# Optimization experiments

Hardware: AMD Instinct MI355X
Metric: run time of the kernel (lower is better)

## Reference

```python
import jax, jax.numpy as jnp
import numpy as np

N, E, H, ED, DD, TD = 40000, 640000, 128, 32, 32, 128
INPUT_CH = 2 * H + ED + DD  # 320


def setup_inputs() -> dict:
    key = jax.random.key(0)
    ks = jax.random.split(key, 14)
    s = 0.02  # param init scale
    return {
        "h": jax.random.normal(ks[0], (N, H), jnp.float32),
        "pos": jax.random.normal(ks[1], (N, 3), jnp.float32),
        "edge_attr": jax.random.normal(ks[2], (E, ED), jnp.float32),
        "dist": jax.random.normal(ks[3], (E, DD), jnp.float32),
        "time_emb": jax.random.normal(ks[4], (1, TD), jnp.float32),
        # time_mlp: SiLU -> Linear(time_dim, 2*hidden)
        "tW": jax.random.normal(ks[5], (TD, 2 * H), jnp.float32) * s,
        "tb": jnp.zeros((2 * H,), jnp.float32),
        # input_lin: Linear(input_ch, hidden)
        "iW": jax.random.normal(ks[6], (INPUT_CH, H), jnp.float32) * s,
        "ib": jnp.zeros((H,), jnp.float32),
        # coord_mlp: Linear(H,H) -> SiLU -> Linear(H,1,bias=False)
        "c1W": jax.random.normal(ks[7], (H, H), jnp.float32) * s,
        "c1b": jnp.zeros((H,), jnp.float32),
        "c2W": jax.random.normal(ks[8], (H, 1), jnp.float32) * s,
        # CoorsNorm learned scale, init 0.01
        "cn_scale": jnp.full((1,), 0.01, jnp.float32),
        "edge_index": jax.random.randint(ks[9], (2, E), 0, N, jnp.int64),
    }


def reference(h, pos, edge_attr, dist, time_emb, tW, tb, iW, ib, c1W, c1b, c2W, cn_scale, edge_index):
    row, col = edge_index[0], edge_index[1]
    # gather edge endpoint features: [E, 2H+ED+DD]
    h_input = jnp.concatenate([h[row], h[col], edge_attr, dist], axis=1)
    # CoorsNorm(scale_init=0.01): normalize relative coords, learned scale
    coord_diff = pos[row] - pos[col]  # [E, 3]
    nrm = jnp.linalg.norm(coord_diff, axis=-1, keepdims=True)
    coord_diff = coord_diff / jnp.clip(nrm, 1e-8) * cn_scale
    # FiLM params from time embedding
    t = jax.nn.silu(time_emb) @ tW + tb  # [1, 2H]
    shift, scale = jnp.split(t, 2, axis=1)
    # input_lin -> LayerNorm (no affine, eps=1e-6) -> modulate
    x = h_input @ iW + ib  # [E, H]
    mu = jnp.mean(x, axis=-1, keepdims=True)
    var = jnp.var(x, axis=-1, keepdims=True)
    x = (x - mu) * jax.lax.rsqrt(var + 1e-6)
    x = x * (1.0 + scale) + shift
    # coord_mlp -> tanh gate
    inv = jnp.tanh(jax.nn.silu(x @ c1W + c1b) @ c2W)  # [E, 1]
    trans = coord_diff * inv  # [E, 3]
    # scatter-add into per-node coordinate updates
    agg = jax.ops.segment_sum(trans, row, num_segments=pos.shape[0])
    return pos + agg
```

## Files before the change

kernel.cpp:

```cpp
#include <hip/hip_runtime.h>
#include <hip/hip_bf16.h>
#include <stdint.h>

#define NN 40000
#define EE 640000
#define HD 128
#define TDIM 128
#define TB 128
#define NTILES (EE / TB)
#define GRID 512

typedef short  s16x8 __attribute__((ext_vector_type(8)));
typedef float  f32x2 __attribute__((ext_vector_type(2)));
typedef float  f32x4 __attribute__((ext_vector_type(4)));
typedef unsigned int u32x4 __attribute__((ext_vector_type(4)));
typedef unsigned short u16;
typedef unsigned int   u32;

#define PSCL 8.0f
#define PDSC 0.125f

__device__ __forceinline__ u32 cvtpk(float lo, float hi) {
  u32 r; asm("v_cvt_pk_bf16_f32 %0, %1, %2" : "=v"(r) : "v"(lo), "v"(hi)); return r;
}
__device__ __forceinline__ u16 f2b(float f) {
  union { float f; u32 u; } x; x.f = f;
  u32 r = x.u + 0x7fffu + ((x.u >> 16) & 1u);
  return (u16)(r >> 16);
}

__global__ void prep_film_kernel(const float* __restrict__ te, const float* __restrict__ tW,
                                 const float* __restrict__ tb, float* __restrict__ film) {
  __shared__ float s[TDIM];
  int t = threadIdx.x;
  if (t < TDIM) { float v = te[t]; s[t] = v * __builtin_amdgcn_rcpf(1.f + __expf(-v)); }
  __syncthreads();
  float acc = tb[t];
  #pragma unroll 8
  for (int k = 0; k < TDIM; ++k) acc = fmaf(s[k], tW[k * 256 + t], acc);
  film[t] = (t >= 128) ? (1.f + acc) : acc;
}

__global__ void prep_weights_kernel(const float* __restrict__ iW,
                                    const float* __restrict__ c1W,
                                    const float* __restrict__ film,
                                    const float* __restrict__ c1b,
                                    u16* __restrict__ wPt,
                                    u16* __restrict__ wadWt,
                                    u16* __restrict__ c1Wt,
                                    float* __restrict__ biasp) {
  int b = blockIdx.x, t = threadIdx.x;
  if (b < 128) {
    int idx = b * 256 + t;
    int c = idx >> 7, k = idx & 127;
    wPt[idx] = f2b(iW[((c >> 7) * 128 + k) * HD + (c & 127)]);
  } else if (b < 160) {
    int idx = (b - 128) * 256 + t;
    int j = idx & 7, l15 = (idx >> 3) & 15, n = (idx >> 7) & 7, lg = (idx >> 10) & 3, ks = idx >> 12;
    int row = n * 16 + l15;
    int k = ks * 32 + lg * 8 + j;
    wadWt[idx] = f2b(iW[(256 + k) * HD + row]);
  } else if (b < 224) {
    int idx = (b - 160) * 256 + t;
    int j = idx & 7, l15 = (idx >> 3) & 15, n = (idx >> 7) & 7, lg = (idx >> 10) & 3, kq = idx >> 12;
    int row = n * 16 + l15;
    int ch = (kq * 2 + (j >> 2)) * 16 + lg * 4 + (j & 3);
    c1Wt[idx] = f2b(film[128 + ch] * c1W[ch * HD + row]);
  } else if (t < 128) {
    float acc = c1b[t];
    #pragma unroll 8
    for (int k = 0; k < 128; ++k) acc = fmaf(film[k], c1W[k * HD + t], acc);
    biasp[t] = acc;
  }
}

__global__ __launch_bounds__(256) void prep_P_kernel(const float* __restrict__ h,
                                                     const u16* __restrict__ wPt,
                                                     const float* __restrict__ ib,
                                                     const float* __restrict__ pos,
                                                     u32* __restrict__ P,
                                                     float* __restrict__ out) {
  __shared__ u16 sWp[256][136];
  __shared__ float sib[HD];
  int t = threadIdx.x;
  {
    int ci = blockIdx.x * 192 + t;
    if (t < 192) out[ci] = pos[ci];
  }
  if (t < 128) sib[t] = ib[t];
  {
    const u16* src = wPt + t * 128;
    #pragma unroll
    for (int i = 0; i < 16; ++i)
      *(uint4*)&sWp[t][i * 8] = *(const uint4*)(src + i * 8);
  }
  int wave = t >> 6, lane = t & 63, l15 = lane & 15, lg = lane >> 4;
  int node = blockIdx.x * 64 + wave * 16 + l15;
  uint4 hb[4];
  const float* hr = h + (size_t)node * HD + lg * 8;
  #pragma unroll
  for (int c = 0; c < 4; ++c) {
    float4 a = *(const float4*)(hr + c * 32);
    float4 b = *(const float4*)(hr + c * 32 + 4);
    hb[c].x = cvtpk(a.x, a.y); hb[c].y = cvtpk(a.z, a.w);
    hb[c].z = cvtpk(b.x, b.y); hb[c].w = cvtpk(b.z, b.w);
  }
  __syncthreads();
  f32x4 acc[16];
  #pragma unroll
  for (int n = 0; n < 16; ++n) acc[n] = (f32x4){0.f, 0.f, 0.f, 0.f};
  #pragma unroll
  for (int c = 0; c < 4; ++c) {
    s16x8 bF = *(const s16x8*)&hb[c];
    #pragma unroll
    for (int n = 0; n < 16; ++n) {
      s16x8 aF = *(const s16x8*)&sWp[n * 16 + l15][c * 32 + lg * 8];
      acc[n] = __builtin_amdgcn_mfma_f32_16x16x32_bf16(aF, bF, acc[n], 0, 0, 0);
    }
  }
  u32* dst = P + (size_t)node * 64;
  #pragma unroll
  for (int n = 0; n < 16; ++n) {
    int side = n >> 3;
    int cb = (n & 7) * 16 + lg * 4;
    float a0 = acc[n][0], a1 = acc[n][1], a2 = acc[n][2], a3 = acc[n][3];
    if (side == 0) { a0 += sib[cb]; a1 += sib[cb + 1]; a2 += sib[cb + 2]; a3 += sib[cb + 3]; }
    u32 w = __builtin_amdgcn_cvt_pk_fp8_f32(PSCL * a0, PSCL * a1, 0, false);
    w = __builtin_amdgcn_cvt_pk_fp8_f32(PSCL * a2, PSCL * a3, w, true);
    dst[side * 32 + lg * 8 + (n & 7)] = w;
  }
}

struct PfS {
  int ri, ci;
  float4 a0, a1, d0, d1;
  float p0x, p0y, p0z, p1x, p1y, p1z;
};

__global__ __launch_bounds__(512, 4) void edge_kernel(
    const float* __restrict__ pos,
    const float* __restrict__ edge_attr,
    const float* __restrict__ dist,
    const float* __restrict__ c2w,
    const float* __restrict__ cn_scale,
    const int*   __restrict__ eidx,
    const u32*   __restrict__ P,
    const u16*   __restrict__ wadWt,
    const u16*   __restrict__ c1Wt,
    const float* __restrict__ biasp,
    float*       __restrict__ out)
{
  __shared__ u16   sW1[8192];
  __shared__ u16   sW2[16384];
  __shared__ float sC1b[HD];
  __shared__ float sC2w[HD];

  const int t    = threadIdx.x;
  const int lane = t & 63;
  const int wave = t >> 6;
  const int l15  = lane & 15;
  const int lg   = lane >> 4;
  const int wv   = wave * 16 + l15;

  if (t < HD) { sC1b[t] = biasp[t]; sC2w[t] = c2w[t]; }
  {
    const uint4* s1 = (const uint4*)wadWt;
    uint4* d1 = (uint4*)sW1;
    #pragma unroll
    for (int i = 0; i < 2; ++i) d1[t + i * 512] = s1[t + i * 512];
    const uint4* s2 = (const uint4*)c1Wt;
    uint4* d2 = (uint4*)sW2;
    #pragma unroll
    for (int i = 0; i < 4; ++i) d2[t + i * 512] = s2[t + i * 512];
  }

  const float cns = cn_scale[0];
  const int bbase = lg * 2048 + l15 * 16;

  auto pf_idx_ad = [&](PfS& p, int tile) {
    int e = tile * TB + wv;
    p.ri = eidx[e];
    p.ci = eidx[EE + e];
    const float* pa = edge_attr + (size_t)e * 32 + lg * 8;
    const float* pd = dist      + (size_t)e * 32 + lg * 8;
    p.a0 = *(const float4*)(pa); p.a1 = *(const float4*)(pa + 4);
    p.d0 = *(const float4*)(pd); p.d1 = *(const float4*)(pd + 4);
  };
  auto pf_pos = [&](PfS& p) {
    p.p0x = pos[p.ri * 3 + 0]; p.p0y = pos[p.ri * 3 + 1]; p.p0z = pos[p.ri * 3 + 2];
    p.p1x = pos[p.ci * 3 + 0]; p.p1y = pos[p.ci * 3 + 1]; p.p1z = pos[p.ci * 3 + 2];
  };

  PfS A, B;
  pf_idx_ad(A, blockIdx.x);
  pf_pos(A);

  uint4 pra0, pra1, pca0, pca1;
  {
    const u32* pr = P + (size_t)A.ri * 64 + lg * 8;
    const u32* pc = P + (size_t)A.ci * 64 + 32 + lg * 8;
    pra0 = *(const uint4*)(pr); pra1 = *(const uint4*)(pr + 4);
    pca0 = *(const uint4*)(pc); pca1 = *(const uint4*)(pc + 4);
  }

  __syncthreads();

  for (int tile = blockIdx.x; tile < NTILES; tile += GRID) {
    int tn = tile + GRID; if (tn >= NTILES) tn = tile;

    pf_idx_ad(B, tn);

    uint4 ef0, ef1;
    ef0.x = cvtpk(A.a0.x, A.a0.y); ef0.y = cvtpk(A.a0.z, A.a0.w);
    ef0.z = cvtpk(A.a1.x, A.a1.y); ef0.w = cvtpk(A.a1.z, A.a1.w);
    ef1.x = cvtpk(A.d0.x, A.d0.y); ef1.y = cvtpk(A.d0.z, A.d0.w);
    ef1.z = cvtpk(A.d1.x, A.d1.y); ef1.w = cvtpk(A.d1.z, A.d1.w);

    f32x4 acc[8];
    #pragma unroll
    for (int n = 0; n < 8; ++n) acc[n] = (f32x4){0.f, 0.f, 0.f, 0.f};
    #pragma unroll
    for (int ks = 0; ks < 2; ++ks) {
      s16x8 bF = (ks == 0) ? *(const s16x8*)&ef0 : *(const s16x8*)&ef1;
      #pragma unroll
      for (int n = 0; n < 8; ++n) {
        s16x8 aF = *(const s16x8*)((const char*)sW1 + ks * 8192 + bbase + n * 256);
        acc[n] = __builtin_amdgcn_mfma_f32_16x16x32_bf16(aF, bF, acc[n], 0, 0, 0);
      }
    }

    float x[8][4];
    float s0=0.f,s1=0.f,s2=0.f,s3=0.f, q0=0.f,q1=0.f,q2=0.f,q3=0.f;
    #pragma unroll
    for (int i = 0; i < 2; ++i) {
      uint4 wa = (i == 0) ? pra0 : pra1;
      uint4 wc = (i == 0) ? pca0 : pca1;
      #pragma unroll
      for (int k = 0; k < 4; ++k) {
        int n = i * 4 + k;
        u32 aw = (k == 0) ? wa.x : (k == 1) ? wa.y : (k == 2) ? wa.z : wa.w;
        u32 cw = (k == 0) ? wc.x : (k == 1) ? wc.y : (k == 2) ? wc.z : wc.w;
        f32x2 a01 = __builtin_amdgcn_cvt_pk_f32_fp8(aw, false);
        f32x2 a23 = __builtin_amdgcn_cvt_pk_f32_fp8(aw, true);
        f32x2 c01 = __builtin_amdgcn_cvt_pk_f32_fp8(cw, false);
        f32x2 c23 = __builtin_amdgcn_cvt_pk_f32_fp8(cw, true);
        float v0 = fmaf(a01[0] + c01[0], PDSC, acc[n][0]);
        float v1 = fmaf(a01[1] + c01[1], PDSC, acc[n][1]);
        float v2 = fmaf(a23[0] + c23[0], PDSC, acc[n][2]);
        float v3 = fmaf(a23[1] + c23[1], PDSC, acc[n][3]);
        x[n][0] = v0; x[n][1] = v1; x[n][2] = v2; x[n][3] = v3;
        s0 += v0; s1 += v1; s2 += v2; s3 += v3;
        q0 = fmaf(v0,v0,q0); q1 = fmaf(v1,v1,q1);
        q2 = fmaf(v2,v2,q2); q3 = fmaf(v3,v3,q3);
      }
    }
    float sum = (s0 + s1) + (s2 + s3);
    float sq  = (q0 + q1) + (q2 + q3);
    sum += __shfl_xor(sum, 16); sum += __shfl_xor(sum, 32);
    sq  += __shfl_xor(sq,  16); sq  += __shfl_xor(sq,  32);
    float mean = sum * (1.f / 128.f);
    float var  = sq  * (1.f / 128.f) - mean * mean;
    float LA = rsqrtf(var + 1e-6f);
    float LB = -mean * LA;

    union { uint2 u2[8]; u32 w[16]; } xb;
    #pragma unroll
    for (int n = 0; n < 8; ++n) {
      float y0 = fmaf(x[n][0], LA, LB);
      float y1 = fmaf(x[n][1], LA, LB);
      float y2 = fmaf(x[n][2], LA, LB);
      float y3 = fmaf(x[n][3], LA, LB);
      xb.u2[n].x = cvtpk(y0, y1);
      xb.u2[n].y = cvtpk(y2, y3);
    }

    #pragma unroll
    for (int n = 0; n < 8; ++n) acc[n] = (f32x4){0.f, 0.f, 0.f, 0.f};
    #pragma unroll
    for (int kq = 0; kq < 4; ++kq) {
      u32x4 xw = { xb.w[4*kq], xb.w[4*kq+1], xb.w[4*kq+2], xb.w[4*kq+3] };
      s16x8 xF = __builtin_bit_cast(s16x8, xw);
      #pragma unroll
      for (int n = 0; n < 8; ++n) {
        s16x8 aF = *(const s16x8*)((const char*)sW2 + kq * 8192 + bbase + n * 256);
        acc[n] = __builtin_amdgcn_mfma_f32_16x16x32_bf16(aF, xF, acc[n], 0, 0, 0);
      }
    }

    float z0=0.f, z1=0.f, z2=0.f, z3=0.f;
    #pragma unroll
    for (int n = 0; n < 8; ++n) {
      int cb = n * 16 + lg * 4;
      f32x4 cb4 = *(const f32x4*)&sC1b[cb];
      f32x4 cw4 = *(const f32x4*)&sC2w[cb];
      float y0 = acc[n][0] + cb4[0];
      float y1 = acc[n][1] + cb4[1];
      float y2 = acc[n][2] + cb4[2];
      float y3 = acc[n][3] + cb4[3];
      z0 = fmaf(y0 * __builtin_amdgcn_rcpf(1.f + __expf(-y0)), cw4[0], z0);
      z1 = fmaf(y1 * __builtin_amdgcn_rcpf(1.f + __expf(-y1)), cw4[1], z1);
      z2 = fmaf(y2 * __builtin_amdgcn_rcpf(1.f + __expf(-y2)), cw4[2], z2);
      z3 = fmaf(y3 * __builtin_amdgcn_rcpf(1.f + __expf(-y3)), cw4[3], z3);
    }
    float z = (z0 + z1) + (z2 + z3);
    z += __shfl_xor(z, 16); z += __shfl_xor(z, 32);

    pf_pos(B);
    uint4 qra0, qra1, qca0, qca1;
    {
      const u32* pr = P + (size_t)B.ri * 64 + lg * 8;
      const u32* pc = P + (size_t)B.ci * 64 + 32 + lg * 8;
      qra0 = *(const uint4*)(pr); qra1 = *(const uint4*)(pr + 4);
      qca0 = *(const uint4*)(pc); qca1 = *(const uint4*)(pc + 4);
    }

    if (lg < 3) {
      float zc = fminf(fmaxf(z, -15.f), 15.f);
      float ez = __expf(2.f * zc);
      float inv = (ez - 1.f) * __builtin_amdgcn_rcpf(ez + 1.f);
      float dx = A.p0x - A.p1x, dy = A.p0y - A.p1y, dz = A.p0z - A.p1z;
      float nrm = sqrtf(fmaf(dx, dx, fmaf(dy, dy, dz * dz)));
      float sc  = cns * inv * __builtin_amdgcn_rcpf(fmaxf(nrm, 1e-8f));
      float d   = (lg == 0) ? dx : ((lg == 1) ? dy : dz);
      atomicAdd(out + (size_t)A.ri * 3 + lg, d * sc);
    }

    A = B;
    pra0 = qra0; pra1 = qra1;
    pca0 = qca0; pca1 = qca1;
  }
}

extern "C" void kernel_launch(void* const* d_in, const int* in_sizes, int n_in,
                              void* d_out, int out_size, void* d_ws, size_t ws_size,
                              hipStream_t stream) {
  const float* h         = (const float*)d_in[0];
  const float* pos       = (const float*)d_in[1];
  const float* edge_attr = (const float*)d_in[2];
  const float* dist      = (const float*)d_in[3];
  const float* te        = (const float*)d_in[4];
  const float* tW        = (const float*)d_in[5];
  const float* tb        = (const float*)d_in[6];
  const float* iW        = (const float*)d_in[7];
  const float* ib        = (const float*)d_in[8];
  const float* c1W       = (const float*)d_in[9];
  const float* c1b       = (const float*)d_in[10];
  const float* c2W       = (const float*)d_in[11];
  const float* cn        = (const float*)d_in[12];
  const int*   eidx      = (const int*)d_in[13];
  float* out = (float*)d_out;

  char* ws = (char*)d_ws;
  u32*   P      = (u32*)(ws);
  u16*   wPt    = (u16*)(ws + 10240000);
  u16*   wadWt  = (u16*)(ws + 10305536);
  u16*   c1Wt   = (u16*)(ws + 10321920);
  float* film   = (float*)(ws + 10354688);
  float* biasp  = (float*)(ws + 10355712);

  hipLaunchKernelGGL(prep_film_kernel,    dim3(1),    dim3(256), 0, stream, te, tW, tb, film);
  hipLaunchKernelGGL(prep_weights_kernel, dim3(225),  dim3(256), 0, stream,
                     iW, c1W, film, c1b, wPt, wadWt, c1Wt, biasp);
  hipLaunchKernelGGL(prep_P_kernel,       dim3(625),  dim3(256), 0, stream,
                     h, wPt, ib, pos, P, out);
  hipLaunchKernelGGL(edge_kernel,         dim3(GRID), dim3(512), 0, stream,
                     pos, edge_attr, dist, c2W, cn, eidx,
                     P, wadWt, c1Wt, biasp, out);
}
```

Baseline: 99.61 us.

## Switch edge MLP matmuls from bf16 to fp8 MFMA with scaled weights

Converts the edge-attribute/dist projection and the coord_mlp first layer to fp8 (e4m3) MFMA, storing weights pre-scaled by 16 in fp8 and undoing the scale after accumulation. This halves weight LDS footprint and operand register width, aiming to cut MFMA and LDS cost per edge. The grid is also raised from 512 to 768 blocks to use the freed LDS for more resident blocks. The cost is extra quantization error on the activations and weights.

```diff
diff --git a/kernel.cpp b/kernel.cpp
--- a/kernel.cpp
+++ b/kernel.cpp
@@ -8,17 +8,18 @@
 #define TDIM 128
 #define TB 128
 #define NTILES (EE / TB)
-#define GRID 512
+#define GRID 768
 
 typedef short  s16x8 __attribute__((ext_vector_type(8)));
 typedef float  f32x2 __attribute__((ext_vector_type(2)));
 typedef float  f32x4 __attribute__((ext_vector_type(4)));
-typedef unsigned int u32x4 __attribute__((ext_vector_type(4)));
 typedef unsigned short u16;
 typedef unsigned int   u32;
 
 #define PSCL 8.0f
 #define PDSC 0.125f
+#define WSCALE 16.0f
+#define WDSC 0.0625f
 
 __device__ __forceinline__ u32 cvtpk(float lo, float hi) {
   u32 r; asm("v_cvt_pk_bf16_f32 %0, %1, %2" : "=v"(r) : "v"(lo), "v"(hi)); return r;
@@ -54,18 +55,27 @@
     int idx = b * 256 + t;
     int c = idx >> 7, k = idx & 127;
     wPt[idx] = f2b(iW[((c >> 7) * 128 + k) * HD + (c & 127)]);
-  } else if (b < 160) {
-    int idx = (b - 128) * 256 + t;
-    int j = idx & 7, l15 = (idx >> 3) & 15, n = (idx >> 7) & 7, lg = (idx >> 10) & 3, ks = idx >> 12;
+  } else if (b < 144) {
+    int pidx = (b - 128) * 256 + t;
+    int idx = pidx * 2;
+    int j0 = idx & 7, l15 = (idx >> 3) & 15, n = (idx >> 7) & 7, lg = (idx >> 10) & 3, ks = idx >> 12;
     int row = n * 16 + l15;
-    int k = ks * 32 + lg * 8 + j;
-    wadWt[idx] = f2b(iW[(256 + k) * HD + row]);
-  } else if (b < 224) {
-    int idx = (b - 160) * 256 + t;
-    int j = idx & 7, l15 = (idx >> 3) & 15, n = (idx >> 7) & 7, lg = (idx >> 10) & 3, kq = idx >> 12;
+    int k0 = ks * 32 + lg * 8 + j0;
+    float v0 = WSCALE * iW[(256 + k0) * HD + row];
+    float v1 = WSCALE * iW[(256 + k0 + 1) * HD + row];
+    u32 p = __builtin_amdgcn_cvt_pk_fp8_f32(v0, v1, 0, false);
+    wadWt[pidx] = (u16)p;
+  } else if (b < 176) {
+    int pidx = (b - 144) * 256 + t;
+    int idx = pidx * 2;
+    int j0 = idx & 7, l15 = (idx >> 3) & 15, n = (idx >> 7) & 7, lg = (idx >> 10) & 3, kq = idx >> 12;
     int row = n * 16 + l15;
-    int ch = (kq * 2 + (j >> 2)) * 16 + lg * 4 + (j & 3);
-    c1Wt[idx] = f2b(film[128 + ch] * c1W[ch * HD + row]);
+    int ch0 = (kq * 2 + (j0 >> 2)) * 16 + lg * 4 + (j0 & 3);
+    int ch1 = (kq * 2 + ((j0 + 1) >> 2)) * 16 + lg * 4 + ((j0 + 1) & 3);
+    float v0 = WSCALE * film[128 + ch0] * c1W[ch0 * HD + row];
+    float v1 = WSCALE * film[128 + ch1] * c1W[ch1 * HD + row];
+    u32 p = __builtin_amdgcn_cvt_pk_fp8_f32(v0, v1, 0, false);
+    c1Wt[pidx] = (u16)p;
   } else if (t < 128) {
     float acc = c1b[t];
     #pragma unroll 8
@@ -150,8 +160,8 @@
     const float* __restrict__ biasp,
     float*       __restrict__ out)
 {
-  __shared__ u16   sW1[8192];
-  __shared__ u16   sW2[16384];
+  __shared__ u16   sW1[4096];
+  __shared__ u16   sW2[8192];
   __shared__ float sC1b[HD];
   __shared__ float sC2w[HD];
 
@@ -166,16 +176,15 @@
   {
     const uint4* s1 = (const uint4*)wadWt;
     uint4* d1 = (uint4*)sW1;
-    #pragma unroll
-    for (int i = 0; i < 2; ++i) d1[t + i * 512] = s1[t + i * 512];
+    if (t < 512) d1[t] = s1[t];
     const uint4* s2 = (const uint4*)c1Wt;
     uint4* d2 = (uint4*)sW2;
     #pragma unroll
-    for (int i = 0; i < 4; ++i) d2[t + i * 512] = s2[t + i * 512];
+    for (int i = 0; i < 2; ++i) d2[t + i * 512] = s2[t + i * 512];
   }
 
   const float cns = cn_scale[0];
-  const int bbase = lg * 2048 + l15 * 16;
+  const int bb8 = lg * 1024 + l15 * 8;
 
   auto pf_idx_ad = [&](PfS& p, int tile) {
     int e = tile * TB + wv;
@@ -210,22 +219,30 @@
 
     pf_idx_ad(B, tn);
 
-    uint4 ef0, ef1;
-    ef0.x = cvtpk(A.a0.x, A.a0.y); ef0.y = cvtpk(A.a0.z, A.a0.w);
-    ef0.z = cvtpk(A.a1.x, A.a1.y); ef0.w = cvtpk(A.a1.z, A.a1.w);
-    ef1.x = cvtpk(A.d0.x, A.d0.y); ef1.y = cvtpk(A.d0.z, A.d0.w);
-    ef1.z = cvtpk(A.d1.x, A.d1.y); ef1.w = cvtpk(A.d1.z, A.d1.w);
+    long ef0, ef1;
+    {
+      u32 a0 = __builtin_amdgcn_cvt_pk_fp8_f32(A.a0.x, A.a0.y, 0, false);
+      a0 = __builtin_amdgcn_cvt_pk_fp8_f32(A.a0.z, A.a0.w, a0, true);
+      u32 a1 = __builtin_amdgcn_cvt_pk_fp8_f32(A.a1.x, A.a1.y, 0, false);
+      a1 = __builtin_amdgcn_cvt_pk_fp8_f32(A.a1.z, A.a1.w, a1, true);
+      u32 d0 = __builtin_amdgcn_cvt_pk_fp8_f32(A.d0.x, A.d0.y, 0, false);
+      d0 = __builtin_amdgcn_cvt_pk_fp8_f32(A.d0.z, A.d0.w, d0, true);
+      u32 d1 = __builtin_amdgcn_cvt_pk_fp8_f32(A.d1.x, A.d1.y, 0, false);
+      d1 = __builtin_amdgcn_cvt_pk_fp8_f32(A.d1.z, A.d1.w, d1, true);
+      ef0 = (long)(((unsigned long long)a1 << 32) | a0);
+      ef1 = (long)(((unsigned long long)d1 << 32) | d0);
+    }
 
     f32x4 acc[8];
     #pragma unroll
     for (int n = 0; n < 8; ++n) acc[n] = (f32x4){0.f, 0.f, 0.f, 0.f};
     #pragma unroll
     for (int ks = 0; ks < 2; ++ks) {
-      s16x8 bF = (ks == 0) ? *(const s16x8*)&ef0 : *(const s16x8*)&ef1;
+      long bF = (ks == 0) ? ef0 : ef1;
       #pragma unroll
       for (int n = 0; n < 8; ++n) {
-        s16x8 aF = *(const s16x8*)((const char*)sW1 + ks * 8192 + bbase + n * 256);
-        acc[n] = __builtin_amdgcn_mfma_f32_16x16x32_bf16(aF, bF, acc[n], 0, 0, 0);
+        long aF = *(const long*)((const char*)sW1 + ks * 4096 + bb8 + n * 128);
+        acc[n] = __builtin_amdgcn_mfma_f32_16x16x32_fp8_fp8(aF, bF, acc[n], 0, 0, 0);
       }
     }
 
@@ -244,10 +261,10 @@
         f32x2 a23 = __builtin_amdgcn_cvt_pk_f32_fp8(aw, true);
         f32x2 c01 = __builtin_amdgcn_cvt_pk_f32_fp8(cw, false);
         f32x2 c23 = __builtin_amdgcn_cvt_pk_f32_fp8(cw, true);
-        float v0 = fmaf(a01[0] + c01[0], PDSC, acc[n][0]);
-        float v1 = fmaf(a01[1] + c01[1], PDSC, acc[n][1]);
-        float v2 = fmaf(a23[0] + c23[0], PDSC, acc[n][2]);
-        float v3 = fmaf(a23[1] + c23[1], PDSC, acc[n][3]);
+        float v0 = fmaf(acc[n][0], WDSC, (a01[0] + c01[0]) * PDSC);
+        float v1 = fmaf(acc[n][1], WDSC, (a01[1] + c01[1]) * PDSC);
+        float v2 = fmaf(acc[n][2], WDSC, (a23[0] + c23[0]) * PDSC);
+        float v3 = fmaf(acc[n][3], WDSC, (a23[1] + c23[1]) * PDSC);
         x[n][0] = v0; x[n][1] = v1; x[n][2] = v2; x[n][3] = v3;
         s0 += v0; s1 += v1; s2 += v2; s3 += v3;
         q0 = fmaf(v0,v0,q0); q1 = fmaf(v1,v1,q1);
@@ -263,27 +280,27 @@
     float LA = rsqrtf(var + 1e-6f);
     float LB = -mean * LA;
 
-    union { uint2 u2[8]; u32 w[16]; } xb;
+    u32 xp[8];
     #pragma unroll
     for (int n = 0; n < 8; ++n) {
       float y0 = fmaf(x[n][0], LA, LB);
       float y1 = fmaf(x[n][1], LA, LB);
       float y2 = fmaf(x[n][2], LA, LB);
       float y3 = fmaf(x[n][3], LA, LB);
-      xb.u2[n].x = cvtpk(y0, y1);
-      xb.u2[n].y = cvtpk(y2, y3);
+      u32 w = __builtin_amdgcn_cvt_pk_fp8_f32(y0, y1, 0, false);
+      w = __builtin_amdgcn_cvt_pk_fp8_f32(y2, y3, w, true);
+      xp[n] = w;
     }
 
     #pragma unroll
     for (int n = 0; n < 8; ++n) acc[n] = (f32x4){0.f, 0.f, 0.f, 0.f};
     #pragma unroll
     for (int kq = 0; kq < 4; ++kq) {
-      u32x4 xw = { xb.w[4*kq], xb.w[4*kq+1], xb.w[4*kq+2], xb.w[4*kq+3] };
-      s16x8 xF = __builtin_bit_cast(s16x8, xw);
+      long xF = (long)(((unsigned long long)xp[2*kq+1] << 32) | xp[2*kq]);
       #pragma unroll
       for (int n = 0; n < 8; ++n) {
-        s16x8 aF = *(const s16x8*)((const char*)sW2 + kq * 8192 + bbase + n * 256);
-        acc[n] = __builtin_amdgcn_mfma_f32_16x16x32_bf16(aF, xF, acc[n], 0, 0, 0);
+        long aF = *(const long*)((const char*)sW2 + kq * 4096 + bb8 + n * 128);
+        acc[n] = __builtin_amdgcn_mfma_f32_16x16x32_fp8_fp8(aF, xF, acc[n], 0, 0, 0);
       }
     }
 
@@ -293,10 +310,10 @@
       int cb = n * 16 + lg * 4;
       f32x4 cb4 = *(const f32x4*)&sC1b[cb];
       f32x4 cw4 = *(const f32x4*)&sC2w[cb];
-      float y0 = acc[n][0] + cb4[0];
-      float y1 = acc[n][1] + cb4[1];
-      float y2 = acc[n][2] + cb4[2];
-      float y3 = acc[n][3] + cb4[3];
+      float y0 = fmaf(acc[n][0], WDSC, cb4[0]);
+      float y1 = fmaf(acc[n][1], WDSC, cb4[1]);
+      float y2 = fmaf(acc[n][2], WDSC, cb4[2]);
+      float y3 = fmaf(acc[n][3], WDSC, cb4[3]);
       z0 = fmaf(y0 * __builtin_amdgcn_rcpf(1.f + __expf(-y0)), cw4[0], z0);
       z1 = fmaf(y1 * __builtin_amdgcn_rcpf(1.f + __expf(-y1)), cw4[1], z1);
       z2 = fmaf(y2 * __builtin_amdgcn_rcpf(1.f + __expf(-y2)), cw4[2], z2);
@@ -354,12 +371,12 @@
   u32*   P      = (u32*)(ws);
   u16*   wPt    = (u16*)(ws + 10240000);
   u16*   wadWt  = (u16*)(ws + 10305536);
-  u16*   c1Wt   = (u16*)(ws + 10321920);
-  float* film   = (float*)(ws + 10354688);
-  float* biasp  = (float*)(ws + 10355712);
+  u16*   c1Wt   = (u16*)(ws + 10313728);
+  float* film   = (float*)(ws + 10330112);
+  float* biasp  = (float*)(ws + 10331136);
 
   hipLaunchKernelGGL(prep_film_kernel,    dim3(1),    dim3(256), 0, stream, te, tW, tb, film);
-  hipLaunchKernelGGL(prep_weights_kernel, dim3(225),  dim3(256), 0, stream,
+  hipLaunchKernelGGL(prep_weights_kernel, dim3(177),  dim3(256), 0, stream,
                      iW, c1W, film, c1b, wPt, wadWt, c1Wt, biasp);
   hipLaunchKernelGGL(prep_P_kernel,       dim3(625),  dim3(256), 0, stream,
                      h, wPt, ib, pos, P, out);
```

Measured after the change: 363.3 us. 265% more time.
